# Optimization experiments

Hardware: AMD Instinct MI355X
Metric: run time of the kernel (lower is better)

The kernel has to match this reference:

```python
import jax, jax.numpy as jnp
import numpy as np

B, D, H, T = 4096, 64, 256, 200

def setup_inputs() -> dict:
    key = jax.random.key(0)
    ks = jax.random.split(key, 4)
    def xavier(k, fan_in, fan_out):
        lim = np.sqrt(6.0 / (fan_in + fan_out)).astype(np.float32)
        return jax.random.uniform(k, (fan_in, fan_out), jnp.float32, -lim, lim)
    return {
        "y0": jax.random.normal(ks[0], (B, D), jnp.float32),
        "t": jnp.arange(T, dtype=jnp.float32) * 0.01,
        "W1": xavier(ks[1], D, H),
        "b1": jnp.zeros((H,), jnp.float32),
        "W2": xavier(ks[2], H, H),
        "b2": jnp.zeros((H,), jnp.float32),
        "W3": xavier(ks[3], H, D),
        "b3": jnp.zeros((D,), jnp.float32),
    }

def reference(y0, t, W1, b1, W2, b2, W3, b3):
    # odeint uses constant dt = t[1] - t[0] (as in the original code)
    dt = t[1] - t[0]
    num_steps = t.shape[0]

    def mlp(y):  # dy/dt = f(y); autonomous, t unused
        h = jax.nn.relu(y @ W1 + b1)
        h = jax.nn.relu(h @ W2 + b2)
        return h @ W3 + b3

    def step(y, _):
        y_new = y + dt * mlp(y)
        return y_new, y_new

    _, ys = jax.lax.scan(step, y0, None, length=num_steps - 1)  # [T-1, B, D]
    # solution: [B, T, D] with solution[:, 0] = y0
    return jnp.concatenate([y0[:, None, :], jnp.transpose(ys, (1, 0, 2))], axis=1)
```

## Files before the change

### kernel.cpp

```cpp
#include <hip/hip_runtime.h>
#include <hip/hip_bf16.h>

#define BATCH   4096
#define DIM     64
#define HID     256
#define TSTEPS  200
#define SROWS   16
#define NBLOCKS (BATCH / SROWS)
#define NTH     512

#define HP  264
#define YPB 72

typedef __bf16 bf16_t;
typedef bf16_t bf16x8 __attribute__((ext_vector_type(8)));
typedef float  f32x4  __attribute__((ext_vector_type(4)));

__device__ __forceinline__ unsigned short f2bf(float f) {
    unsigned u = __builtin_bit_cast(unsigned, f);
    u += 0x7FFFu + ((u >> 16) & 1u);
    return (unsigned short)(u >> 16);
}

#if __has_builtin(__builtin_amdgcn_cvt_pk_bf16_f32)
__device__ __forceinline__ unsigned pk2(float lo, float hi) {
    return __builtin_bit_cast(unsigned, __builtin_amdgcn_cvt_pk_bf16_f32(lo, hi));
}
#else
__device__ __forceinline__ unsigned pk2(float lo, float hi) {
    return (unsigned)f2bf(lo) | ((unsigned)f2bf(hi) << 16);
}
#endif


__global__ void prep_weights(const float* __restrict__ W1,
                             const float* __restrict__ W2,
                             const float* __restrict__ W3,
                             unsigned short* __restrict__ ws) {
    int u = blockIdx.x * blockDim.x + threadIdx.x;
    if (u >= 12288) return;
    const int lane = u & 63, l16 = lane & 15, quad = lane >> 4;
    const float* src; int ld, m, kk; bool perm;
    if (u < 2048) {
        int r = u >> 6; kk = r & 1; int mt = r >> 1;
        src = W1; ld = 256; m = mt * 16 + l16; perm = false;
    } else if (u < 10240) {
        int r = (u - 2048) >> 6; kk = r & 7; int mt = r >> 3;
        src = W2; ld = 256; m = mt * 16 + l16; perm = true;
    } else {
        int r = (u - 10240) >> 6; kk = r & 7; int mt = r >> 3;
        src = W3; ld = 64;  m = mt * 16 + l16; perm = true;
    }
    unsigned short tmp[8] __attribute__((aligned(16)));
    #pragma unroll
    for (int j = 0; j < 8; ++j) {
        int k = perm ? kk * 32 + ((j >> 2) << 4) + quad * 4 + (j & 3)
                     : kk * 32 + quad * 8 + j;
        tmp[j] = f2bf(src[(size_t)k * ld + m]);
    }
    *(uint4*)(ws + (size_t)u * 8) = *(const uint4*)tmp;
}

__global__ void __launch_bounds__(NTH, 2)
ode_kernel(const float* __restrict__ y0,
           const float* __restrict__ tarr,
           const float* __restrict__ b1,
           const float* __restrict__ b2,
           const float* __restrict__ b3,
           const unsigned short* __restrict__ wf,
           float* __restrict__ out) {
    __shared__ __align__(16) unsigned short ybt[SROWS * YPB];
    __shared__ __align__(16) unsigned short h1s[SROWS * HP];
    __shared__ __align__(16) unsigned short h2s[SROWS * HP];

    const int tid  = threadIdx.x;
    const int w    = tid >> 6;
    const int lane = tid & 63;
    const int l16  = lane & 15;
    const int quad = lane >> 4;
    const int b0   = blockIdx.x * SROWS;

    const float dt = tarr[1] - tarr[0];

    const bf16x8* wv = (const bf16x8*)wf;
    bf16x8 w1f[2][2], w2f[2][8], w3f[8];
    #pragma unroll
    for (int mt = 0; mt < 2; ++mt) {
        const int g = w * 2 + mt;
        #pragma unroll
        for (int kk = 0; kk < 2; ++kk) w1f[mt][kk] = wv[(g * 2 + kk) * 64 + lane];
        #pragma unroll
        for (int kk = 0; kk < 8; ++kk) w2f[mt][kk] = wv[2048 + (g * 8 + kk) * 64 + lane];
    }
    if (w < 4)
        #pragma unroll
        for (int kk = 0; kk < 8; ++kk) w3f[kk] = wv[10240 + (w * 8 + kk) * 64 + lane];

    f32x4 binit1[2], binit2[2], binit3;
    #pragma unroll
    for (int mt = 0; mt < 2; ++mt)
        #pragma unroll
        for (int r = 0; r < 4; ++r) {
            binit1[mt][r] = b1[w * 32 + mt * 16 + quad * 4 + r];
            binit2[mt][r] = b2[w * 32 + mt * 16 + quad * 4 + r];
        }

    float yreg[4];
    float* outp = out;
    if (w < 4) {
        #pragma unroll
        for (int r = 0; r < 4; ++r) binit3[r] = b3[w * 16 + quad * 4 + r];
        outp = out + (size_t)(b0 + l16) * (TSTEPS * DIM) + w * 16 + quad * 4;
        float4 v = *(const float4*)&y0[(size_t)(b0 + l16) * DIM + w * 16 + quad * 4];
        yreg[0] = v.x; yreg[1] = v.y; yreg[2] = v.z; yreg[3] = v.w;
        uint2 p; p.x = pk2(v.x, v.y); p.y = pk2(v.z, v.w);
        *(uint2*)&ybt[l16 * YPB + w * 16 + quad * 4] = p;
        *(float4*)outp = v;
        outp += DIM;
    }
    __syncthreads();

    const unsigned short* ybase  = &ybt[l16 * YPB];
    const unsigned short* h1base = &h1s[l16 * HP];
    const unsigned short* h2base = &h2s[l16 * HP];
    const int ep_off = l16 * HP + w * 32 + quad * 8;

    for (int t = 1; t < TSTEPS; ++t) {
        {
            f32x4 acc[2] = {binit1[0], binit1[1]};
            bf16x8 bfr[2];
            #pragma unroll
            for (int kk = 0; kk < 2; ++kk)
                bfr[kk] = *(const bf16x8*)&ybase[kk * 32 + quad * 8];
            #pragma unroll
            for (int kk = 0; kk < 2; ++kk)
                #pragma unroll
                for (int mt = 0; mt < 2; ++mt)
                    acc[mt] = __builtin_amdgcn_mfma_f32_16x16x32_bf16(
                        w1f[mt][kk], bfr[kk], acc[mt], 0, 0, 0);
            uint4 p;
            p.x = pk2(acc[0][0] > 0.f ? acc[0][0] : 0.f, acc[0][1] > 0.f ? acc[0][1] : 0.f);
            p.y = pk2(acc[0][2] > 0.f ? acc[0][2] : 0.f, acc[0][3] > 0.f ? acc[0][3] : 0.f);
            p.z = pk2(acc[1][0] > 0.f ? acc[1][0] : 0.f, acc[1][1] > 0.f ? acc[1][1] : 0.f);
            p.w = pk2(acc[1][2] > 0.f ? acc[1][2] : 0.f, acc[1][3] > 0.f ? acc[1][3] : 0.f);
            *(uint4*)&h1s[ep_off] = p;
        }
        __syncthreads();

        {
            f32x4 acc[2] = {binit2[0], binit2[1]};
            bf16x8 bfr[8];
            #pragma unroll
            for (int kk = 0; kk < 8; ++kk)
                bfr[kk] = *(const bf16x8*)&h1base[kk * 32 + quad * 8];
            #pragma unroll
            for (int kk = 0; kk < 8; ++kk)
                #pragma unroll
                for (int mt = 0; mt < 2; ++mt)
                    acc[mt] = __builtin_amdgcn_mfma_f32_16x16x32_bf16(
                        w2f[mt][kk], bfr[kk], acc[mt], 0, 0, 0);
            uint4 p;
            p.x = pk2(acc[0][0] > 0.f ? acc[0][0] : 0.f, acc[0][1] > 0.f ? acc[0][1] : 0.f);
            p.y = pk2(acc[0][2] > 0.f ? acc[0][2] : 0.f, acc[0][3] > 0.f ? acc[0][3] : 0.f);
            p.z = pk2(acc[1][0] > 0.f ? acc[1][0] : 0.f, acc[1][1] > 0.f ? acc[1][1] : 0.f);
            p.w = pk2(acc[1][2] > 0.f ? acc[1][2] : 0.f, acc[1][3] > 0.f ? acc[1][3] : 0.f);
            *(uint4*)&h2s[ep_off] = p;
        }
        __syncthreads();

        if (w < 4) {
            f32x4 accA = binit3;
            f32x4 accB = {0.f, 0.f, 0.f, 0.f};
            bf16x8 bfr[8];
            #pragma unroll
            for (int kk = 0; kk < 8; ++kk)
                bfr[kk] = *(const bf16x8*)&h2base[kk * 32 + quad * 8];
            #pragma unroll
            for (int k = 0; k < 4; ++k) {
                accA = __builtin_amdgcn_mfma_f32_16x16x32_bf16(
                    w3f[k], bfr[k], accA, 0, 0, 0);
                accB = __builtin_amdgcn_mfma_f32_16x16x32_bf16(
                    w3f[k + 4], bfr[k + 4], accB, 0, 0, 0);
            }
            f32x4 acc = accA + accB;
            #pragma unroll
            for (int r = 0; r < 4; ++r)
                yreg[r] = __builtin_fmaf(dt, acc[r], yreg[r]);
            uint2 p; p.x = pk2(yreg[0], yreg[1]); p.y = pk2(yreg[2], yreg[3]);
            *(uint2*)&ybt[l16 * YPB + w * 16 + quad * 4] = p;
            float4 ov; ov.x = yreg[0]; ov.y = yreg[1]; ov.z = yreg[2]; ov.w = yreg[3];
            *(float4*)outp = ov;
            outp += DIM;
        }
        __syncthreads();
    }
}

extern "C" void kernel_launch(void* const* d_in, const int* in_sizes, int n_in,
                              void* d_out, int out_size, void* d_ws, size_t ws_size,
                              hipStream_t stream) {
    const float* y0 = (const float*)d_in[0];
    const float* t  = (const float*)d_in[1];
    const float* W1 = (const float*)d_in[2];
    const float* b1 = (const float*)d_in[3];
    const float* W2 = (const float*)d_in[4];
    const float* b2 = (const float*)d_in[5];
    const float* W3 = (const float*)d_in[6];
    const float* b3 = (const float*)d_in[7];
    float* out = (float*)d_out;
    unsigned short* wf = (unsigned short*)d_ws;

    prep_weights<<<48, 256, 0, stream>>>(W1, W2, W3, wf);
    ode_kernel<<<NBLOCKS, NTH, 0, stream>>>(y0, t, b1, b2, b3, wf, out);
}
```

Before: 384.0 us.

## Fold W3·W1 into a recurrence on the first-layer pre-activation

The first-layer pre-activation z = y·W1 + b1 now evolves by linearity as z_{t+1} = z_t + h2·(dt·W3·W1) + dt·b3·W1. The product matrix and bias vector are precomputed in the weight-prep kernel, which removes the per-step layer-1 matmul and one barrier per step. The layer-1 work is merged into the layer-3 phase, where all 8 waves now do the 256x256 product while 4 waves still compute y for the output. The cost is more MFMAs per step (a K=256 product instead of K=64) and more weight registers. Accuracy also changes, because z accumulates in fp32 across steps instead of being recomputed from a bf16-rounded y.

After: 390.4 us. About the same (+1.7%).

```diff
diff --git a/kernel.cpp b/kernel.cpp
--- a/kernel.cpp
+++ b/kernel.cpp
@@ -10,7 +10,10 @@
 #define NTH     512
 
 #define HP  264
-#define YPB 72
+
+#define SLOT_W3   8192
+#define SLOT_W31  10240
+#define SLOT_END  18432
 
 typedef __bf16 bf16_t;
 typedef bf16_t bf16x8 __attribute__((ext_vector_type(8)));
@@ -32,44 +35,68 @@
 }
 #endif
 
-
 __global__ void prep_weights(const float* __restrict__ W1,
                              const float* __restrict__ W2,
                              const float* __restrict__ W3,
+                             const float* __restrict__ b3,
+                             const float* __restrict__ tarr,
                              unsigned short* __restrict__ ws) {
     int u = blockIdx.x * blockDim.x + threadIdx.x;
-    if (u >= 12288) return;
-    const int lane = u & 63, l16 = lane & 15, quad = lane >> 4;
-    const float* src; int ld, m, kk; bool perm;
-    if (u < 2048) {
-        int r = u >> 6; kk = r & 1; int mt = r >> 1;
-        src = W1; ld = 256; m = mt * 16 + l16; perm = false;
-    } else if (u < 10240) {
-        int r = (u - 2048) >> 6; kk = r & 7; int mt = r >> 3;
-        src = W2; ld = 256; m = mt * 16 + l16; perm = true;
-    } else {
-        int r = (u - 10240) >> 6; kk = r & 7; int mt = r >> 3;
-        src = W3; ld = 64;  m = mt * 16 + l16; perm = true;
-    }
-    unsigned short tmp[8] __attribute__((aligned(16)));
-    #pragma unroll
-    for (int j = 0; j < 8; ++j) {
-        int k = perm ? kk * 32 + ((j >> 2) << 4) + quad * 4 + (j & 3)
-                     : kk * 32 + quad * 8 + j;
-        tmp[j] = f2bf(src[(size_t)k * ld + m]);
-    }
-    *(uint4*)(ws + (size_t)u * 8) = *(const uint4*)tmp;
+    const float dt = tarr[1] - tarr[0];
+    if (u < SLOT_W31) {
+        const int lane = u & 63, l16 = lane & 15, quad = lane >> 4;
+        const float* src; int ld, m, kk;
+        if (u < SLOT_W3) {
+            int r = u >> 6; kk = r & 7; int g = r >> 3;
+            src = W2; ld = HID; m = g * 16 + l16;
+        } else {
+            int r = (u - SLOT_W3) >> 6; kk = r & 7; int g = r >> 3;
+            src = W3; ld = DIM; m = g * 16 + l16;
+        }
+        unsigned short tmp[8] __attribute__((aligned(16)));
+        #pragma unroll
+        for (int j = 0; j < 8; ++j) {
+            int k = kk * 32 + ((j >> 2) << 4) + quad * 4 + (j & 3);
+            tmp[j] = f2bf(src[(size_t)k * ld + m]);
+        }
+        *(uint4*)(ws + (size_t)u * 8) = *(const uint4*)tmp;
+    } else if (u < SLOT_END) {
+        const int lane = u & 63, l16 = lane & 15, quad = lane >> 4;
+        int r = (u - SLOT_W31) >> 6; int kk = r & 7; int g = r >> 3;
+        int m = g * 16 + l16;
+        float acc[8] = {0.f, 0.f, 0.f, 0.f, 0.f, 0.f, 0.f, 0.f};
+        int kj[8];
+        #pragma unroll
+        for (int j = 0; j < 8; ++j)
+            kj[j] = kk * 32 + ((j >> 2) << 4) + quad * 4 + (j & 3);
+        for (int d = 0; d < DIM; ++d) {
+            float w1v = W1[(size_t)d * HID + m];
+            #pragma unroll
+            for (int j = 0; j < 8; ++j)
+                acc[j] = __builtin_fmaf(W3[(size_t)kj[j] * DIM + d], w1v, acc[j]);
+        }
+        unsigned short tmp[8] __attribute__((aligned(16)));
+        #pragma unroll
+        for (int j = 0; j < 8; ++j) tmp[j] = f2bf(dt * acc[j]);
+        *(uint4*)(ws + (size_t)u * 8) = *(const uint4*)tmp;
+    } else if (u < SLOT_END + HID) {
+        int h = u - SLOT_END;
+        float a = 0.f;
+        for (int d = 0; d < DIM; ++d)
+            a = __builtin_fmaf(b3[d], W1[(size_t)d * HID + h], a);
+        ((float*)(ws + (size_t)SLOT_END * 8))[h] = dt * a;
+    }
 }
 
 __global__ void __launch_bounds__(NTH, 2)
 ode_kernel(const float* __restrict__ y0,
            const float* __restrict__ tarr,
+           const float* __restrict__ W1,
            const float* __restrict__ b1,
            const float* __restrict__ b2,
            const float* __restrict__ b3,
            const unsigned short* __restrict__ wf,
            float* __restrict__ out) {
-    __shared__ __align__(16) unsigned short ybt[SROWS * YPB];
     __shared__ __align__(16) unsigned short h1s[SROWS * HP];
     __shared__ __align__(16) unsigned short h2s[SROWS * HP];
 
@@ -83,26 +110,28 @@
     const float dt = tarr[1] - tarr[0];
 
     const bf16x8* wv = (const bf16x8*)wf;
-    bf16x8 w1f[2][2], w2f[2][8], w3f[8];
+    bf16x8 w2f[2][8], w31f[2][8], w3f[8];
     #pragma unroll
     for (int mt = 0; mt < 2; ++mt) {
         const int g = w * 2 + mt;
         #pragma unroll
-        for (int kk = 0; kk < 2; ++kk) w1f[mt][kk] = wv[(g * 2 + kk) * 64 + lane];
-        #pragma unroll
-        for (int kk = 0; kk < 8; ++kk) w2f[mt][kk] = wv[2048 + (g * 8 + kk) * 64 + lane];
+        for (int kk = 0; kk < 8; ++kk) {
+            w2f[mt][kk]  = wv[(g * 8 + kk) * 64 + lane];
+            w31f[mt][kk] = wv[SLOT_W31 + (g * 8 + kk) * 64 + lane];
+        }
     }
     if (w < 4)
         #pragma unroll
-        for (int kk = 0; kk < 8; ++kk) w3f[kk] = wv[10240 + (w * 8 + kk) * 64 + lane];
-
-    f32x4 binit1[2], binit2[2], binit3;
+        for (int kk = 0; kk < 8; ++kk) w3f[kk] = wv[SLOT_W3 + (w * 8 + kk) * 64 + lane];
+
+    f32x4 binit2[2], dtb31[2], binit3;
+    const float* vb31 = (const float*)(wf + (size_t)SLOT_END * 8);
     #pragma unroll
     for (int mt = 0; mt < 2; ++mt)
         #pragma unroll
         for (int r = 0; r < 4; ++r) {
-            binit1[mt][r] = b1[w * 32 + mt * 16 + quad * 4 + r];
-            binit2[mt][r] = b2[w * 32 + mt * 16 + quad * 4 + r];
+            binit2[mt][r] = b2[(w * 2 + mt) * 16 + quad * 4 + r];
+            dtb31[mt][r]  = vb31[(w * 2 + mt) * 16 + quad * 4 + r];
         }
 
     float yreg[4];
@@ -114,39 +143,49 @@
         float4 v = *(const float4*)&y0[(size_t)(b0 + l16) * DIM + w * 16 + quad * 4];
         yreg[0] = v.x; yreg[1] = v.y; yreg[2] = v.z; yreg[3] = v.w;
         uint2 p; p.x = pk2(v.x, v.y); p.y = pk2(v.z, v.w);
-        *(uint2*)&ybt[l16 * YPB + w * 16 + quad * 4] = p;
+        *(uint2*)&h2s[l16 * HP + w * 16 + quad * 4] = p;
         *(float4*)outp = v;
         outp += DIM;
     }
     __syncthreads();
 
-    const unsigned short* ybase  = &ybt[l16 * YPB];
     const unsigned short* h1base = &h1s[l16 * HP];
     const unsigned short* h2base = &h2s[l16 * HP];
     const int ep_off = l16 * HP + w * 32 + quad * 8;
 
+    f32x4 zacc[2];
+    {
+        bf16x8 ybfr[2];
+        #pragma unroll
+        for (int kk = 0; kk < 2; ++kk)
+            ybfr[kk] = *(const bf16x8*)&h2s[l16 * HP + kk * 32 + quad * 8];
+        #pragma unroll
+        for (int mt = 0; mt < 2; ++mt) {
+            f32x4 a;
+            #pragma unroll
+            for (int r = 0; r < 4; ++r) a[r] = b1[(w * 2 + mt) * 16 + quad * 4 + r];
+            #pragma unroll
+            for (int kk = 0; kk < 2; ++kk) {
+                unsigned short t8[8] __attribute__((aligned(16)));
+                #pragma unroll
+                for (int j = 0; j < 8; ++j)
+                    t8[j] = f2bf(W1[(size_t)(kk * 32 + quad * 8 + j) * HID
+                                    + (w * 2 + mt) * 16 + l16]);
+                bf16x8 wf1 = *(const bf16x8*)t8;
+                a = __builtin_amdgcn_mfma_f32_16x16x32_bf16(wf1, ybfr[kk], a, 0, 0, 0);
+            }
+            zacc[mt] = a;
+        }
+        uint4 p;
+        p.x = pk2(zacc[0][0] > 0.f ? zacc[0][0] : 0.f, zacc[0][1] > 0.f ? zacc[0][1] : 0.f);
+        p.y = pk2(zacc[0][2] > 0.f ? zacc[0][2] : 0.f, zacc[0][3] > 0.f ? zacc[0][3] : 0.f);
+        p.z = pk2(zacc[1][0] > 0.f ? zacc[1][0] : 0.f, zacc[1][1] > 0.f ? zacc[1][1] : 0.f);
+        p.w = pk2(zacc[1][2] > 0.f ? zacc[1][2] : 0.f, zacc[1][3] > 0.f ? zacc[1][3] : 0.f);
+        *(uint4*)&h1s[ep_off] = p;
+    }
+    __syncthreads();
+
     for (int t = 1; t < TSTEPS; ++t) {
-        {
-            f32x4 acc[2] = {binit1[0], binit1[1]};
-            bf16x8 bfr[2];
-            #pragma unroll
-            for (int kk = 0; kk < 2; ++kk)
-                bfr[kk] = *(const bf16x8*)&ybase[kk * 32 + quad * 8];
-            #pragma unroll
-            for (int kk = 0; kk < 2; ++kk)
-                #pragma unroll
-                for (int mt = 0; mt < 2; ++mt)
-                    acc[mt] = __builtin_amdgcn_mfma_f32_16x16x32_bf16(
-                        w1f[mt][kk], bfr[kk], acc[mt], 0, 0, 0);
-            uint4 p;
-            p.x = pk2(acc[0][0] > 0.f ? acc[0][0] : 0.f, acc[0][1] > 0.f ? acc[0][1] : 0.f);
-            p.y = pk2(acc[0][2] > 0.f ? acc[0][2] : 0.f, acc[0][3] > 0.f ? acc[0][3] : 0.f);
-            p.z = pk2(acc[1][0] > 0.f ? acc[1][0] : 0.f, acc[1][1] > 0.f ? acc[1][1] : 0.f);
-            p.w = pk2(acc[1][2] > 0.f ? acc[1][2] : 0.f, acc[1][3] > 0.f ? acc[1][3] : 0.f);
-            *(uint4*)&h1s[ep_off] = p;
-        }
-        __syncthreads();
-
         {
             f32x4 acc[2] = {binit2[0], binit2[1]};
             bf16x8 bfr[8];
@@ -168,29 +207,44 @@
         }
         __syncthreads();
 
-        if (w < 4) {
-            f32x4 accA = binit3;
-            f32x4 accB = {0.f, 0.f, 0.f, 0.f};
+        {
             bf16x8 bfr[8];
             #pragma unroll
             for (int kk = 0; kk < 8; ++kk)
                 bfr[kk] = *(const bf16x8*)&h2base[kk * 32 + quad * 8];
             #pragma unroll
-            for (int k = 0; k < 4; ++k) {
-                accA = __builtin_amdgcn_mfma_f32_16x16x32_bf16(
-                    w3f[k], bfr[k], accA, 0, 0, 0);
-                accB = __builtin_amdgcn_mfma_f32_16x16x32_bf16(
-                    w3f[k + 4], bfr[k + 4], accB, 0, 0, 0);
+            for (int kk = 0; kk < 8; ++kk) {
+                zacc[0] = __builtin_amdgcn_mfma_f32_16x16x32_bf16(
+                    w31f[0][kk], bfr[kk], zacc[0], 0, 0, 0);
+                zacc[1] = __builtin_amdgcn_mfma_f32_16x16x32_bf16(
+                    w31f[1][kk], bfr[kk], zacc[1], 0, 0, 0);
             }
-            f32x4 acc = accA + accB;
-            #pragma unroll
-            for (int r = 0; r < 4; ++r)
-                yreg[r] = __builtin_fmaf(dt, acc[r], yreg[r]);
-            uint2 p; p.x = pk2(yreg[0], yreg[1]); p.y = pk2(yreg[2], yreg[3]);
-            *(uint2*)&ybt[l16 * YPB + w * 16 + quad * 4] = p;
-            float4 ov; ov.x = yreg[0]; ov.y = yreg[1]; ov.z = yreg[2]; ov.w = yreg[3];
-            *(float4*)outp = ov;
-            outp += DIM;
+            if (w < 4) {
+                f32x4 ya = binit3;
+                f32x4 yb = {0.f, 0.f, 0.f, 0.f};
+                #pragma unroll
+                for (int k = 0; k < 4; ++k) {
+                    ya = __builtin_amdgcn_mfma_f32_16x16x32_bf16(
+                        w3f[k], bfr[k], ya, 0, 0, 0);
+                    yb = __builtin_amdgcn_mfma_f32_16x16x32_bf16(
+                        w3f[k + 4], bfr[k + 4], yb, 0, 0, 0);
+                }
+                f32x4 ys = ya + yb;
+                #pragma unroll
+                for (int r = 0; r < 4; ++r)
+                    yreg[r] = __builtin_fmaf(dt, ys[r], yreg[r]);
+                float4 ov; ov.x = yreg[0]; ov.y = yreg[1]; ov.z = yreg[2]; ov.w = yreg[3];
+                *(float4*)outp = ov;
+                outp += DIM;
+            }
+            zacc[0] += dtb31[0];
+            zacc[1] += dtb31[1];
+            uint4 p;
+            p.x = pk2(zacc[0][0] > 0.f ? zacc[0][0] : 0.f, zacc[0][1] > 0.f ? zacc[0][1] : 0.f);
+            p.y = pk2(zacc[0][2] > 0.f ? zacc[0][2] : 0.f, zacc[0][3] > 0.f ? zacc[0][3] : 0.f);
+            p.z = pk2(zacc[1][0] > 0.f ? zacc[1][0] : 0.f, zacc[1][1] > 0.f ? zacc[1][1] : 0.f);
+            p.w = pk2(zacc[1][2] > 0.f ? zacc[1][2] : 0.f, zacc[1][3] > 0.f ? zacc[1][3] : 0.f);
+            *(uint4*)&h1s[ep_off] = p;
         }
         __syncthreads();
     }
@@ -210,6 +264,6 @@
     float* out = (float*)d_out;
     unsigned short* wf = (unsigned short*)d_ws;
 
-    prep_weights<<<48, 256, 0, stream>>>(W1, W2, W3, wf);
-    ode_kernel<<<NBLOCKS, NTH, 0, stream>>>(y0, t, b1, b2, b3, wf, out);
-}
+    prep_weights<<<73, 256, 0, stream>>>(W1, W2, W3, b3, t, wf);
+    ode_kernel<<<NBLOCKS, NTH, 0, stream>>>(y0, t, W1, b1, b2, b3, wf, out);
+}
```
